# Performance work log

Measured on AMD Instinct MI355X. Metric: run time of the kernel, lower is better.

The kernel has to match this reference:

```python
import jax, jax.numpy as jnp
import numpy as np

NUM_HEADS = 8
EPS = 1e-6


def setup_inputs() -> dict:
    key = jax.random.key(0)
    ks = jax.random.split(key, 6)
    B, T, E = 2, 4096, 512
    s = 0.02
    x = jax.random.normal(ks[0], (B, T, E), dtype=jnp.float32)
    Wq = jax.random.normal(ks[1], (E, E), dtype=jnp.float32) * s
    Wk = jax.random.normal(ks[2], (E, E), dtype=jnp.float32) * s
    Wv = jax.random.normal(ks[3], (E, E), dtype=jnp.float32) * s
    Wo = jax.random.normal(ks[4], (E, E), dtype=jnp.float32) * s
    bq = jnp.zeros((E,), jnp.float32)
    bk = jnp.zeros((E,), jnp.float32)
    bv = jnp.zeros((E,), jnp.float32)
    bo = jnp.zeros((E,), jnp.float32)
    return {"x": x, "Wq": Wq, "bq": bq, "Wk": Wk, "bk": bk,
            "Wv": Wv, "bv": bv, "Wo": Wo, "bo": bo}


def _linear(x, W, b):
    # torch nn.Linear: y = x @ W.T + b
    return x @ W.T + b


def _feature_map(x):
    return jax.nn.elu(x) + 1.0


def _linear_attention(x, Wq, bq, Wk, bk, Wv, bv, Wo, bo):
    B, T, E = x.shape
    H = NUM_HEADS
    D = E // H

    def heads(y):  # (B,T,E) -> (T,B,H,D), time-major for scan
        return y.reshape(B, T, H, D).transpose(1, 0, 2, 3)

    q = _feature_map(heads(_linear(x, Wq, bq)))
    k = _feature_map(heads(_linear(x, Wk, bk)))
    v = heads(_linear(x, Wv, bv))

    # Causal linear attention: running KV outer-product state S (B,H,D,D)
    # and running key sum z (B,H,D). Equivalent to the naive
    # cumsum-of-outer-products (B,H,T,D,D) formulation, but O(D^2) state.
    S0 = jnp.zeros((B, H, D, D), x.dtype)
    z0 = jnp.zeros((B, H, D), x.dtype)

    def step(carry, qkv):
        S, z = carry
        qt, kt, vt = qkv  # each (B,H,D)
        S = S + kt[..., :, None] * vt[..., None, :]
        z = z + kt
        num = jnp.einsum('bhd,bhde->bhe', qt, S)
        den = jnp.sum(qt * z, axis=-1) + EPS  # (B,H)
        return (S, z), num / den[..., None]

    _, out = jax.lax.scan(step, (S0, z0), (q, k, v))  # (T,B,H,D)
    out = out.transpose(1, 0, 2, 3).reshape(B, T, E)
    return _linear(out, Wo, bo)


def reference(x, Wq, bq, Wk, bk, Wv, bv, Wo, bo):
    return _linear_attention(x, Wq, bq, Wk, bk, Wv, bv, Wo, bo)
```

## Files before the change

### kernel.cpp

```cpp
#include <hip/hip_runtime.h>
#include <hip/hip_bf16.h>

#define T_SEQ 4096
#define EMB   512
#define NH    8
#define HD    64
#define BATCH 2
#define M_ROWS (BATCH * T_SEQ)
#define NCHUNK 64
#define CS     64
#define BHEADS (BATCH * NH)

using bf16 = __hip_bfloat16;
typedef __attribute__((ext_vector_type(8))) short short8;
typedef __attribute__((ext_vector_type(4))) float floatx4;

__device__ __forceinline__ float bs2f(short s) {
    return __uint_as_float(((unsigned)(unsigned short)s) << 16);
}
__device__ __forceinline__ short f2bs(float f) {
    bf16 h = __float2bfloat16(f);
    return *reinterpret_cast<short*>(&h);
}
__device__ __forceinline__ float load_elem(const bf16* p, size_t i) {
    return __bfloat162float(p[i]);
}
__device__ __forceinline__ void store_elem(bf16* p, size_t i, float v) {
    p[i] = __float2bfloat16(v);
}
__device__ __forceinline__ void store_elem(float* p, size_t i, float v) {
    p[i] = v;
}
__device__ __forceinline__ void stage8(const bf16* g, short* l) {
    *reinterpret_cast<short8*>(l) = *reinterpret_cast<const short8*>(g);
}
__device__ __forceinline__ void stage8(const float* g, short* l) {
    float4 a = *reinterpret_cast<const float4*>(g);
    float4 b = *reinterpret_cast<const float4*>(g + 4);
    short8 v;
    v[0] = f2bs(a.x); v[1] = f2bs(a.y); v[2] = f2bs(a.z); v[3] = f2bs(a.w);
    v[4] = f2bs(b.x); v[5] = f2bs(b.y); v[6] = f2bs(b.z); v[7] = f2bs(b.w);
    *reinterpret_cast<short8*>(l) = v;
}
template <typename T> struct ModeOf { static constexpr int v = 0; };
template <> struct ModeOf<float>    { static constexpr int v = 1; };

__device__ __forceinline__ void gload_lds16(const short* g, short* l) {
    __builtin_amdgcn_global_load_lds(
        (const __attribute__((address_space(1))) void*)g,
        (__attribute__((address_space(3))) void*)l, 16, 0, 0);
}

#define LDSTR 72

__global__ void detect_dtype(const unsigned short* __restrict__ xraw,
                             int* __restrict__ flag)
{
    __shared__ int bad_s;
    const int tid = threadIdx.x;
    if (tid == 0) bad_s = 0;
    __syncthreads();
    bool bad = false;
    #pragma unroll
    for (int i = 0; i < 2; ++i) {
        uint4 u = reinterpret_cast<const uint4*>(xraw)[tid + i * 256];
        const unsigned w[4] = {u.x, u.y, u.z, u.w};
        #pragma unroll
        for (int k = 0; k < 4; ++k) {
            const float f = __uint_as_float(w[k] << 16);
            if (!(fabsf(f) <= 1e9f)) bad = true;
        }
    }
    if (bad) atomicOr(&bad_s, 1);
    __syncthreads();
    if (tid == 0) *flag = bad_s ? 1 : 0;
}

template <typename T>
__global__ __launch_bounds__(256) void convert_all(
    const int* __restrict__ flag,
    const T* __restrict__ x,
    const T* __restrict__ Wq, const T* __restrict__ bq,
    const T* __restrict__ Wk, const T* __restrict__ bk,
    const T* __restrict__ Wv, const T* __restrict__ bv,
    const T* __restrict__ Wo, const T* __restrict__ bo,
    short* __restrict__ xb, short* __restrict__ Wb, short* __restrict__ bb)
{
    if (*flag != ModeOf<T>::v) return;
    const int c = blockIdx.x * 256 + threadIdx.x;
    if (c < 524288) {
        stage8(x + (size_t)c * 8, xb + (size_t)c * 8);
    } else if (c < 655360) {
        const int c2 = c - 524288;
        const int w = c2 >> 15;
        const int off = (c2 & 32767) * 8;
        const T* src = (w == 0) ? Wq : (w == 1) ? Wk : (w == 2) ? Wv : Wo;
        stage8(src + off, Wb + w * 262144 + off);
    } else {
        const int c3 = c - 655360;
        const int bsel = c3 >> 6;
        const int off = (c3 & 63) * 8;
        const T* src = (bsel == 0) ? bq : (bsel == 1) ? bk : (bsel == 2) ? bv : bo;
        stage8(src + off, bb + bsel * 512 + off);
    }
}

__global__ __launch_bounds__(256) void qkv_gemm_dl(
    const short* __restrict__ xb, const short* __restrict__ Wb,
    const short* __restrict__ bb,
    bf16* __restrict__ Qf, bf16* __restrict__ Kf, bf16* __restrict__ Vf)
{
    const int mtile = blockIdx.x;
    const int ntile = blockIdx.y;
    const int which = ntile >> 2;
    const short* W = Wb + (size_t)which * 262144;
    const bf16* bias = (const bf16*)(bb + which * 512);
    bf16* outp = (which == 0) ? Qf : ((which == 1) ? Kf : Vf);
    const int nbase = (ntile & 3) * 128;
    const int mbase = mtile * 128;

    __shared__ short As[128 * 64];
    __shared__ short Bs[128 * 64];

    const int tid  = threadIdx.x;
    const int wave = tid >> 6, lane = tid & 63;
    const int wm = wave >> 1, wn = wave & 1;
    const int lm = lane & 15, quad = lane >> 4;
    const int srow = lane >> 3;
    const int scol = (lane & 7) * 8;

    floatx4 acc[4][4];
    const floatx4 zero = {0.f, 0.f, 0.f, 0.f};
    #pragma unroll
    for (int mt = 0; mt < 4; ++mt)
        #pragma unroll
        for (int nt = 0; nt < 4; ++nt) acc[mt][nt] = zero;

    for (int kt = 0; kt < EMB; kt += 64) {
        #pragma unroll
        for (int j = 0; j < 4; ++j) {
            const int issue = wave * 4 + j;
            const int row = issue * 8 + srow;
            gload_lds16(xb + (size_t)(mbase + row) * EMB + kt + scol,
                        &As[issue * 512]);
            gload_lds16(W  + (size_t)(nbase + row) * EMB + kt + scol,
                        &Bs[issue * 512]);
        }
        __syncthreads();
        #pragma unroll
        for (int ks = 0; ks < 2; ++ks) {
            short8 af[4], bfr[4];
            #pragma unroll
            for (int mt = 0; mt < 4; ++mt)
                af[mt] = *reinterpret_cast<const short8*>(
                    &As[(wm * 64 + mt * 16 + lm) * 64 + ks * 32 + quad * 8]);
            #pragma unroll
            for (int nt = 0; nt < 4; ++nt)
                bfr[nt] = *reinterpret_cast<const short8*>(
                    &Bs[(wn * 64 + nt * 16 + lm) * 64 + ks * 32 + quad * 8]);
            #pragma unroll
            for (int mt = 0; mt < 4; ++mt)
                #pragma unroll
                for (int nt = 0; nt < 4; ++nt)
                    acc[mt][nt] = __builtin_amdgcn_mfma_f32_16x16x32_bf16(
                        af[mt], bfr[nt], acc[mt][nt], 0, 0, 0);
        }
        __syncthreads();
    }

    #pragma unroll
    for (int nt = 0; nt < 4; ++nt) {
        const int col = nbase + wn * 64 + nt * 16 + lm;
        const float bv_ = load_elem(bias, col & 511);
        const int h = col >> 6, d = col & 63;
        #pragma unroll
        for (int mt = 0; mt < 4; ++mt)
            #pragma unroll
            for (int r = 0; r < 4; ++r) {
                const int row = mbase + wm * 64 + mt * 16 + quad * 4 + r;
                const int b = row >> 12, t = row & (T_SEQ - 1);
                float v = acc[mt][nt][r] + bv_;
                if (which != 2) v = (v > 0.f) ? (v + 1.f) : __expf(v);
                outp[(((size_t)(b * NH + h)) * T_SEQ + t) * HD + d] = __float2bfloat16(v);
            }
    }
}

__global__ __launch_bounds__(256) void chunk_kv(
    const bf16* __restrict__ Kf, const bf16* __restrict__ Vf,
    float* __restrict__ KV, float* __restrict__ ksum)
{
    const int bh = blockIdx.x >> 6;
    const int c  = blockIdx.x & 63;
    __shared__ short Kt[64 * LDSTR];
    __shared__ short Vt[64 * LDSTR];
    const int tid = threadIdx.x;
    const bf16* kp = Kf + ((size_t)bh * T_SEQ + c * CS) * HD;
    const bf16* vp = Vf + ((size_t)bh * T_SEQ + c * CS) * HD;

    #pragma unroll
    for (int j = 0; j < 2; ++j) {
        const int u = j * 256 + tid;
        const int e0 = u * 8;
        const int s = e0 >> 6, d0 = e0 & 63;
        short8 ku = *reinterpret_cast<const short8*>(kp + e0);
        short8 vu = *reinterpret_cast<const short8*>(vp + e0);
        #pragma unroll
        for (int i = 0; i < 8; ++i) {
            Kt[(d0 + i) * LDSTR + s] = ku[i];
            Vt[(d0 + i) * LDSTR + s] = vu[i];
        }
    }
    __syncthreads();

    const int w = tid >> 6, lane = tid & 63;
    const int lm = lane & 15, quad = lane >> 4;

    floatx4 acc[4];
    const floatx4 zero = {0.f, 0.f, 0.f, 0.f};
    #pragma unroll
    for (int nt = 0; nt < 4; ++nt) acc[nt] = zero;

    #pragma unroll
    for (int ks = 0; ks < 2; ++ks) {
        short8 ak = *reinterpret_cast<const short8*>(
            &Kt[(w * 16 + lm) * LDSTR + ks * 32 + quad * 8]);
        #pragma unroll
        for (int nt = 0; nt < 4; ++nt) {
            short8 bv = *reinterpret_cast<const short8*>(
                &Vt[(nt * 16 + lm) * LDSTR + ks * 32 + quad * 8]);
            acc[nt] = __builtin_amdgcn_mfma_f32_16x16x32_bf16(ak, bv, acc[nt], 0, 0, 0);
        }
    }

    float* kvout = KV + ((size_t)bh * NCHUNK + c) * 4096;
    #pragma unroll
    for (int nt = 0; nt < 4; ++nt)
        #pragma unroll
        for (int r = 0; r < 4; ++r) {
            const int dk = w * 16 + quad * 4 + r;
            const int dv = nt * 16 + lm;
            kvout[dk * 64 + dv] = acc[nt][r];
        }

    if (tid < 64) {
        float s = 0.f;
        #pragma unroll 8
        for (int t = 0; t < 64; ++t) s += bs2f(Kt[tid * LDSTR + t]);
        ksum[((size_t)bh * NCHUNK + c) * 64 + tid] = s;
    }
}

__global__ __launch_bounds__(256) void prefix_kv(
    float* __restrict__ KV, float* __restrict__ ksum)
{
    const int bh   = blockIdx.x >> 4;
    const int part = blockIdx.x & 15;
    const int tid  = threadIdx.x;
    const int e    = part * 256 + tid;
    float* base = KV + (size_t)bh * NCHUNK * 4096 + e;

    float s = 0.f;
    #pragma unroll
    for (int cb = 0; cb < 4; ++cb) {
        float v[16];
        #pragma unroll
        for (int i = 0; i < 16; ++i) v[i] = base[(size_t)(cb * 16 + i) * 4096];
        #pragma unroll
        for (int i = 0; i < 16; ++i) {
            const float tmp = v[i];
            base[(size_t)(cb * 16 + i) * 4096] = s;
            s += tmp;
        }
    }

    if (part == 0 && tid < 64) {
        float* zb = ksum + (size_t)bh * NCHUNK * 64 + tid;
        float z = 0.f;
        #pragma unroll
        for (int cb = 0; cb < 4; ++cb) {
            float v[16];
            #pragma unroll
            for (int i = 0; i < 16; ++i) v[i] = zb[(size_t)(cb * 16 + i) * 64];
            #pragma unroll
            for (int i = 0; i < 16; ++i) {
                const float tmp = v[i];
                zb[(size_t)(cb * 16 + i) * 64] = z;
                z += tmp;
            }
        }
    }
}

__global__ __launch_bounds__(256) void attn_mfma(
    const bf16* __restrict__ Qf, const bf16* __restrict__ Kf,
    const bf16* __restrict__ Vf, const float* __restrict__ KV,
    const float* __restrict__ ksum, bf16* __restrict__ Of)
{
    const int bh = blockIdx.x >> 6;
    const int c  = blockIdx.x & 63;
    const int b  = bh >> 3, h = bh & 7;

    __shared__ short Qs [64 * LDSTR];
    __shared__ short Ksn[64 * LDSTR];
    __shared__ short Vt [64 * LDSTR];
    __shared__ short Ps [64 * LDSTR];
    __shared__ short St [64 * LDSTR];
    __shared__ float zprev[64];
    __shared__ float rden[64];

    const int tid = threadIdx.x;
    const int w = tid >> 6, lane = tid & 63;
    const int lm = lane & 15, quad = lane >> 4;
    const size_t coff = ((size_t)bh * T_SEQ + c * CS) * HD;
    const float* Sp = KV + ((size_t)bh * NCHUNK + c) * 4096;

    #pragma unroll
    for (int j = 0; j < 2; ++j) {
        const int u  = j * 256 + tid;
        const int e0 = u * 8;
        const int r = e0 >> 6, cc = e0 & 63;
        *reinterpret_cast<short8*>(&Qs [r * LDSTR + cc]) =
            *reinterpret_cast<const short8*>(Qf + coff + e0);
        *reinterpret_cast<short8*>(&Ksn[r * LDSTR + cc]) =
            *reinterpret_cast<const short8*>(Kf + coff + e0);
        short8 vu = *reinterpret_cast<const short8*>(Vf + coff + e0);
        #pragma unroll
        for (int i = 0; i < 8; ++i) Vt[(cc + i) * LDSTR + r] = vu[i];
    }
    #pragma unroll
    for (int j = 0; j < 4; ++j) {
        const int u = j * 256 + tid;
        const float4 s4 = reinterpret_cast<const float4*>(Sp)[u];
        const int d = u >> 4;
        const int dv0 = (u & 15) * 4;
        St[(dv0 + 0) * LDSTR + d] = f2bs(s4.x);
        St[(dv0 + 1) * LDSTR + d] = f2bs(s4.y);
        St[(dv0 + 2) * LDSTR + d] = f2bs(s4.z);
        St[(dv0 + 3) * LDSTR + d] = f2bs(s4.w);
    }
    if (tid < 64) zprev[tid] = ksum[((size_t)bh * NCHUNK + c) * 64 + tid];
    __syncthreads();

    const floatx4 zero = {0.f, 0.f, 0.f, 0.f};
    short8 aq[2];
    #pragma unroll
    for (int ks = 0; ks < 2; ++ks)
        aq[ks] = *reinterpret_cast<const short8*>(
            &Qs[(w * 16 + lm) * LDSTR + ks * 32 + quad * 8]);

    floatx4 pacc[4];
    #pragma unroll
    for (int nt = 0; nt < 4; ++nt) pacc[nt] = zero;
    #pragma unroll
    for (int ks = 0; ks < 2; ++ks)
        #pragma unroll
        for (int nt = 0; nt < 4; ++nt) {
            short8 bk = *reinterpret_cast<const short8*>(
                &Ksn[(nt * 16 + lm) * LDSTR + ks * 32 + quad * 8]);
            pacc[nt] = __builtin_amdgcn_mfma_f32_16x16x32_bf16(aq[ks], bk, pacc[nt], 0, 0, 0);
        }
    #pragma unroll
    for (int nt = 0; nt < 4; ++nt)
        #pragma unroll
        for (int r = 0; r < 4; ++r) {
            const int t = w * 16 + quad * 4 + r;
            const int s = nt * 16 + lm;
            Ps[t * LDSTR + s] = f2bs((s <= t) ? pacc[nt][r] : 0.f);
        }

    floatx4 oacc[4];
    #pragma unroll
    for (int nt = 0; nt < 4; ++nt) oacc[nt] = zero;
    #pragma unroll
    for (int ks = 0; ks < 2; ++ks)
        #pragma unroll
        for (int nt = 0; nt < 4; ++nt) {
            short8 bs = *reinterpret_cast<const short8*>(
                &St[(nt * 16 + lm) * LDSTR + ks * 32 + quad * 8]);
            oacc[nt] = __builtin_amdgcn_mfma_f32_16x16x32_bf16(aq[ks], bs, oacc[nt], 0, 0, 0);
        }
    __syncthreads();

    if (tid < 64) {
        float rs = 0.f;
        #pragma unroll 8
        for (int s = 0; s < 64; ++s) rs += bs2f(Ps[tid * LDSTR + s]);
        float dz = 0.f;
        #pragma unroll 8
        for (int d = 0; d < 64; ++d) dz += bs2f(Qs[tid * LDSTR + d]) * zprev[d];
        rden[tid] = 1.f / (rs + dz + 1e-6f);
    }

    #pragma unroll
    for (int ks = 0; ks < 2; ++ks) {
        short8 ap = *reinterpret_cast<const short8*>(
            &Ps[(w * 16 + lm) * LDSTR + ks * 32 + quad * 8]);
        #pragma unroll
        for (int nt = 0; nt < 4; ++nt) {
            short8 bv = *reinterpret_cast<const short8*>(
                &Vt[(nt * 16 + lm) * LDSTR + ks * 32 + quad * 8]);
            oacc[nt] = __builtin_amdgcn_mfma_f32_16x16x32_bf16(ap, bv, oacc[nt], 0, 0, 0);
        }
    }
    __syncthreads();

    #pragma unroll
    for (int nt = 0; nt < 4; ++nt)
        #pragma unroll
        for (int r = 0; r < 4; ++r) {
            const int t  = w * 16 + quad * 4 + r;
            const int dv = nt * 16 + lm;
            const int tg = c * CS + t;
            Of[((size_t)(b * T_SEQ + tg)) * EMB + h * HD + dv] =
                __float2bfloat16(oacc[nt][r] * rden[t]);
        }
}

template <typename T>
__global__ __launch_bounds__(256) void out_proj_dl(
    const int* __restrict__ flag,
    const short* __restrict__ A, const short* __restrict__ Wb,
    const short* __restrict__ bb, T* __restrict__ out)
{
    if (*flag != ModeOf<T>::v) return;

    const int mbase = blockIdx.x * 128;
    const int nbase = blockIdx.y * 128;
    const short* W = Wb + (size_t)3 * 262144;
    const bf16* bias = (const bf16*)(bb + 3 * 512);

    __shared__ short As[128 * 64];
    __shared__ short Bs[128 * 64];

    const int tid  = threadIdx.x;
    const int wave = tid >> 6, lane = tid & 63;
    const int wm = wave >> 1, wn = wave & 1;
    const int lm = lane & 15, quad = lane >> 4;
    const int srow = lane >> 3;
    const int scol = (lane & 7) * 8;

    floatx4 acc[4][4];
    const floatx4 zero = {0.f, 0.f, 0.f, 0.f};
    #pragma unroll
    for (int mt = 0; mt < 4; ++mt)
        #pragma unroll
        for (int nt = 0; nt < 4; ++nt) acc[mt][nt] = zero;

    for (int kt = 0; kt < EMB; kt += 64) {
        #pragma unroll
        for (int j = 0; j < 4; ++j) {
            const int issue = wave * 4 + j;
            const int row = issue * 8 + srow;
            gload_lds16(A + (size_t)(mbase + row) * EMB + kt + scol,
                        &As[issue * 512]);
            gload_lds16(W + (size_t)(nbase + row) * EMB + kt + scol,
                        &Bs[issue * 512]);
        }
        __syncthreads();
        #pragma unroll
        for (int ks = 0; ks < 2; ++ks) {
            short8 af[4], bfr[4];
            #pragma unroll
            for (int mt = 0; mt < 4; ++mt)
                af[mt] = *reinterpret_cast<const short8*>(
                    &As[(wm * 64 + mt * 16 + lm) * 64 + ks * 32 + quad * 8]);
            #pragma unroll
            for (int nt = 0; nt < 4; ++nt)
                bfr[nt] = *reinterpret_cast<const short8*>(
                    &Bs[(wn * 64 + nt * 16 + lm) * 64 + ks * 32 + quad * 8]);
            #pragma unroll
            for (int mt = 0; mt < 4; ++mt)
                #pragma unroll
                for (int nt = 0; nt < 4; ++nt)
                    acc[mt][nt] = __builtin_amdgcn_mfma_f32_16x16x32_bf16(
                        af[mt], bfr[nt], acc[mt][nt], 0, 0, 0);
        }
        __syncthreads();
    }

    #pragma unroll
    for (int nt = 0; nt < 4; ++nt) {
        const int col = nbase + wn * 64 + nt * 16 + lm;
        const float bv_ = load_elem(bias, col);
        #pragma unroll
        for (int mt = 0; mt < 4; ++mt)
            #pragma unroll
            for (int r = 0; r < 4; ++r) {
                const int row = mbase + wm * 64 + mt * 16 + quad * 4 + r;
                store_elem(out, (size_t)row * EMB + col, acc[mt][nt][r] + bv_);
            }
    }
}

extern "C" void kernel_launch(void* const* d_in, const int* in_sizes, int n_in,
                              void* d_out, int out_size, void* d_ws, size_t ws_size,
                              hipStream_t stream)
{
    int*  flag = (int*)d_ws;
    bf16* Qf = (bf16*)((char*)d_ws + 64);
    bf16* Kf = Qf + 4194304;
    bf16* Vf = Kf + 4194304;
    float* KV = (float*)(Vf + 4194304);
    short* xb = (short*)KV;
    float* ks = KV + 4194304;
    bf16* Of = (bf16*)(ks + 65536);
    short* Wb = (short*)(Of + 4194304);
    short* bb = Wb + 1048576;

    detect_dtype<<<1, 256, 0, stream>>>((const unsigned short*)d_in[0], flag);

    convert_all<bf16><<<dim3(2561), 256, 0, stream>>>(flag,
        (const bf16*)d_in[0],
        (const bf16*)d_in[1], (const bf16*)d_in[2],
        (const bf16*)d_in[3], (const bf16*)d_in[4],
        (const bf16*)d_in[5], (const bf16*)d_in[6],
        (const bf16*)d_in[7], (const bf16*)d_in[8],
        xb, Wb, bb);
    convert_all<float><<<dim3(2561), 256, 0, stream>>>(flag,
        (const float*)d_in[0],
        (const float*)d_in[1], (const float*)d_in[2],
        (const float*)d_in[3], (const float*)d_in[4],
        (const float*)d_in[5], (const float*)d_in[6],
        (const float*)d_in[7], (const float*)d_in[8],
        xb, Wb, bb);

    qkv_gemm_dl<<<dim3(64, 12), 256, 0, stream>>>(xb, Wb, bb, Qf, Kf, Vf);
    chunk_kv<<<dim3(BHEADS * NCHUNK), 256, 0, stream>>>(Kf, Vf, KV, ks);
    prefix_kv<<<dim3(BHEADS * 16), 256, 0, stream>>>(KV, ks);
    attn_mfma<<<dim3(BHEADS * NCHUNK), 256, 0, stream>>>(Qf, Kf, Vf, KV, ks, Of);

    out_proj_dl<bf16><<<dim3(64, 4), 256, 0, stream>>>(flag,
        (const short*)Of, Wb, bb, (bf16*)d_out);
    out_proj_dl<float><<<dim3(64, 4), 256, 0, stream>>>(flag,
        (const short*)Of, Wb, bb, (float*)d_out);
}
```

Measured before the change: 167.2 us.

## Fold dtype probe into kernels, transpose KV state, parallelize denominator

Drops the separate dtype-detect kernel and the duplicate per-dtype convert and out-projection launches by having every block probe the input dtype itself with a block-wide OR. This removes three launches at the cost of redundant probe reads in each block. The chunk KV state is now stored transposed, so the attention kernel can pack it into LDS with vector stores instead of scattered scalar ones. The per-row normalizer is computed across all waves with shuffle reductions rather than by 64 serial threads, which also removes one barrier.

```diff
diff --git a/kernel.cpp b/kernel.cpp
--- a/kernel.cpp
+++ b/kernel.cpp
@@ -13,6 +13,7 @@
 
 using bf16 = __hip_bfloat16;
 typedef __attribute__((ext_vector_type(8))) short short8;
+typedef __attribute__((ext_vector_type(4))) short short4v;
 typedef __attribute__((ext_vector_type(4))) float floatx4;
 
 __device__ __forceinline__ float bs2f(short s) {
@@ -24,12 +25,6 @@
 }
 __device__ __forceinline__ float load_elem(const bf16* p, size_t i) {
     return __bfloat162float(p[i]);
-}
-__device__ __forceinline__ void store_elem(bf16* p, size_t i, float v) {
-    p[i] = __float2bfloat16(v);
-}
-__device__ __forceinline__ void store_elem(float* p, size_t i, float v) {
-    p[i] = v;
 }
 __device__ __forceinline__ void stage8(const bf16* g, short* l) {
     *reinterpret_cast<short8*>(l) = *reinterpret_cast<const short8*>(g);
@@ -42,8 +37,6 @@
     v[4] = f2bs(b.x); v[5] = f2bs(b.y); v[6] = f2bs(b.z); v[7] = f2bs(b.w);
     *reinterpret_cast<short8*>(l) = v;
 }
-template <typename T> struct ModeOf { static constexpr int v = 0; };
-template <> struct ModeOf<float>    { static constexpr int v = 1; };
 
 __device__ __forceinline__ void gload_lds16(const short* g, short* l) {
     __builtin_amdgcn_global_load_lds(
@@ -53,17 +46,13 @@
 
 #define LDSTR 72
 
-__global__ void detect_dtype(const unsigned short* __restrict__ xraw,
-                             int* __restrict__ flag)
-{
-    __shared__ int bad_s;
+__device__ __forceinline__ int probe_mode(const void* x) {
+    const uint4* p = (const uint4*)x;
     const int tid = threadIdx.x;
-    if (tid == 0) bad_s = 0;
-    __syncthreads();
     bool bad = false;
     #pragma unroll
     for (int i = 0; i < 2; ++i) {
-        uint4 u = reinterpret_cast<const uint4*>(xraw)[tid + i * 256];
+        uint4 u = p[tid + i * 256];
         const unsigned w[4] = {u.x, u.y, u.z, u.w};
         #pragma unroll
         for (int k = 0; k < 4; ++k) {
@@ -71,38 +60,41 @@
             if (!(fabsf(f) <= 1e9f)) bad = true;
         }
     }
-    if (bad) atomicOr(&bad_s, 1);
-    __syncthreads();
-    if (tid == 0) *flag = bad_s ? 1 : 0;
+    return __syncthreads_or(bad ? 1 : 0) ? 1 : 0;
 }
 
 template <typename T>
-__global__ __launch_bounds__(256) void convert_all(
-    const int* __restrict__ flag,
-    const T* __restrict__ x,
-    const T* __restrict__ Wq, const T* __restrict__ bq,
-    const T* __restrict__ Wk, const T* __restrict__ bk,
-    const T* __restrict__ Wv, const T* __restrict__ bv,
-    const T* __restrict__ Wo, const T* __restrict__ bo,
-    short* __restrict__ xb, short* __restrict__ Wb, short* __restrict__ bb)
-{
-    if (*flag != ModeOf<T>::v) return;
-    const int c = blockIdx.x * 256 + threadIdx.x;
+__device__ __forceinline__ void convert_body(
+    const void* const* in, short* xb, short* Wb, short* bb, int c)
+{
     if (c < 524288) {
-        stage8(x + (size_t)c * 8, xb + (size_t)c * 8);
+        stage8((const T*)in[0] + (size_t)c * 8, xb + (size_t)c * 8);
     } else if (c < 655360) {
         const int c2 = c - 524288;
         const int w = c2 >> 15;
         const int off = (c2 & 32767) * 8;
-        const T* src = (w == 0) ? Wq : (w == 1) ? Wk : (w == 2) ? Wv : Wo;
+        const T* src = (const T*)in[w == 0 ? 1 : (w == 1 ? 3 : (w == 2 ? 5 : 7))];
         stage8(src + off, Wb + w * 262144 + off);
-    } else {
+    } else if (c < 655616) {
         const int c3 = c - 655360;
         const int bsel = c3 >> 6;
         const int off = (c3 & 63) * 8;
-        const T* src = (bsel == 0) ? bq : (bsel == 1) ? bk : (bsel == 2) ? bv : bo;
+        const T* src = (const T*)in[bsel == 0 ? 2 : (bsel == 1 ? 4 : (bsel == 2 ? 6 : 8))];
         stage8(src + off, bb + bsel * 512 + off);
     }
+}
+
+__global__ __launch_bounds__(256) void convert_all(
+    const void* x, const void* Wq, const void* bq,
+    const void* Wk, const void* bk, const void* Wv, const void* bv,
+    const void* Wo, const void* bo,
+    short* __restrict__ xb, short* __restrict__ Wb, short* __restrict__ bb)
+{
+    const void* in[9] = {x, Wq, bq, Wk, bk, Wv, bv, Wo, bo};
+    const int mode = probe_mode(x);
+    const int c = blockIdx.x * 256 + threadIdx.x;
+    if (mode) convert_body<float>(in, xb, Wb, bb, c);
+    else      convert_body<bf16>(in, xb, Wb, bb, c);
 }
 
 __global__ __launch_bounds__(256) void qkv_gemm_dl(
@@ -188,7 +180,7 @@
 
 __global__ __launch_bounds__(256) void chunk_kv(
     const bf16* __restrict__ Kf, const bf16* __restrict__ Vf,
-    float* __restrict__ KV, float* __restrict__ ksum)
+    float* __restrict__ KVt, float* __restrict__ ksum)
 {
     const int bh = blockIdx.x >> 6;
     const int c  = blockIdx.x & 63;
@@ -223,24 +215,24 @@
 
     #pragma unroll
     for (int ks = 0; ks < 2; ++ks) {
-        short8 ak = *reinterpret_cast<const short8*>(
-            &Kt[(w * 16 + lm) * LDSTR + ks * 32 + quad * 8]);
+        short8 av = *reinterpret_cast<const short8*>(
+            &Vt[(w * 16 + lm) * LDSTR + ks * 32 + quad * 8]);
         #pragma unroll
         for (int nt = 0; nt < 4; ++nt) {
-            short8 bv = *reinterpret_cast<const short8*>(
-                &Vt[(nt * 16 + lm) * LDSTR + ks * 32 + quad * 8]);
-            acc[nt] = __builtin_amdgcn_mfma_f32_16x16x32_bf16(ak, bv, acc[nt], 0, 0, 0);
-        }
-    }
-
-    float* kvout = KV + ((size_t)bh * NCHUNK + c) * 4096;
+            short8 bk = *reinterpret_cast<const short8*>(
+                &Kt[(nt * 16 + lm) * LDSTR + ks * 32 + quad * 8]);
+            acc[nt] = __builtin_amdgcn_mfma_f32_16x16x32_bf16(av, bk, acc[nt], 0, 0, 0);
+        }
+    }
+
+    float* kvout = KVt + ((size_t)bh * NCHUNK + c) * 4096;
     #pragma unroll
     for (int nt = 0; nt < 4; ++nt)
         #pragma unroll
         for (int r = 0; r < 4; ++r) {
-            const int dk = w * 16 + quad * 4 + r;
-            const int dv = nt * 16 + lm;
-            kvout[dk * 64 + dv] = acc[nt][r];
+            const int dv = w * 16 + quad * 4 + r;
+            const int dk = nt * 16 + lm;
+            kvout[dv * 64 + dk] = acc[nt][r];
         }
 
     if (tid < 64) {
@@ -252,13 +244,13 @@
 }
 
 __global__ __launch_bounds__(256) void prefix_kv(
-    float* __restrict__ KV, float* __restrict__ ksum)
+    float* __restrict__ KVt, float* __restrict__ ksum)
 {
     const int bh   = blockIdx.x >> 4;
     const int part = blockIdx.x & 15;
     const int tid  = threadIdx.x;
     const int e    = part * 256 + tid;
-    float* base = KV + (size_t)bh * NCHUNK * 4096 + e;
+    float* base = KVt + (size_t)bh * NCHUNK * 4096 + e;
 
     float s = 0.f;
     #pragma unroll
@@ -294,7 +286,7 @@
 
 __global__ __launch_bounds__(256) void attn_mfma(
     const bf16* __restrict__ Qf, const bf16* __restrict__ Kf,
-    const bf16* __restrict__ Vf, const float* __restrict__ KV,
+    const bf16* __restrict__ Vf, const float* __restrict__ KVt,
     const float* __restrict__ ksum, bf16* __restrict__ Of)
 {
     const int bh = blockIdx.x >> 6;
@@ -307,13 +299,12 @@
     __shared__ short Ps [64 * LDSTR];
     __shared__ short St [64 * LDSTR];
     __shared__ float zprev[64];
-    __shared__ float rden[64];
 
     const int tid = threadIdx.x;
     const int w = tid >> 6, lane = tid & 63;
     const int lm = lane & 15, quad = lane >> 4;
     const size_t coff = ((size_t)bh * T_SEQ + c * CS) * HD;
-    const float* Sp = KV + ((size_t)bh * NCHUNK + c) * 4096;
+    const float* Sp = KVt + ((size_t)bh * NCHUNK + c) * 4096;
 
     #pragma unroll
     for (int j = 0; j < 2; ++j) {
@@ -330,14 +321,13 @@
     }
     #pragma unroll
     for (int j = 0; j < 4; ++j) {
-        const int u = j * 256 + tid;
+        const int u  = j * 256 + tid;
+        const int dv = u >> 4, d0 = (u & 15) * 4;
         const float4 s4 = reinterpret_cast<const float4*>(Sp)[u];
-        const int d = u >> 4;
-        const int dv0 = (u & 15) * 4;
-        St[(dv0 + 0) * LDSTR + d] = f2bs(s4.x);
-        St[(dv0 + 1) * LDSTR + d] = f2bs(s4.y);
-        St[(dv0 + 2) * LDSTR + d] = f2bs(s4.z);
-        St[(dv0 + 3) * LDSTR + d] = f2bs(s4.w);
+        short4v pk;
+        pk[0] = f2bs(s4.x); pk[1] = f2bs(s4.y);
+        pk[2] = f2bs(s4.z); pk[3] = f2bs(s4.w);
+        *reinterpret_cast<short4v*>(&St[dv * LDSTR + d0]) = pk;
     }
     if (tid < 64) zprev[tid] = ksum[((size_t)bh * NCHUNK + c) * 64 + tid];
     __syncthreads();
@@ -360,14 +350,34 @@
                 &Ksn[(nt * 16 + lm) * LDSTR + ks * 32 + quad * 8]);
             pacc[nt] = __builtin_amdgcn_mfma_f32_16x16x32_bf16(aq[ks], bk, pacc[nt], 0, 0, 0);
         }
+
+    float tot[4] = {0.f, 0.f, 0.f, 0.f};
     #pragma unroll
     for (int nt = 0; nt < 4; ++nt)
         #pragma unroll
         for (int r = 0; r < 4; ++r) {
             const int t = w * 16 + quad * 4 + r;
             const int s = nt * 16 + lm;
-            Ps[t * LDSTR + s] = f2bs((s <= t) ? pacc[nt][r] : 0.f);
-        }
+            const float m = (s <= t) ? pacc[nt][r] : 0.f;
+            Ps[t * LDSTR + s] = f2bs(m);
+            tot[r] += m;
+        }
+    #pragma unroll
+    for (int r = 0; r < 4; ++r) {
+        const int t = w * 16 + quad * 4 + r;
+        #pragma unroll
+        for (int j = 0; j < 4; ++j) {
+            const int d = lm + j * 16;
+            tot[r] += bs2f(Qs[t * LDSTR + d]) * zprev[d];
+        }
+    }
+    #pragma unroll
+    for (int mask = 1; mask < 16; mask <<= 1)
+        #pragma unroll
+        for (int r = 0; r < 4; ++r) tot[r] += __shfl_xor(tot[r], mask);
+    float rdenl[4];
+    #pragma unroll
+    for (int r = 0; r < 4; ++r) rdenl[r] = 1.f / (tot[r] + 1e-6f);
 
     floatx4 oacc[4];
     #pragma unroll
@@ -382,16 +392,6 @@
         }
     __syncthreads();
 
-    if (tid < 64) {
-        float rs = 0.f;
-        #pragma unroll 8
-        for (int s = 0; s < 64; ++s) rs += bs2f(Ps[tid * LDSTR + s]);
-        float dz = 0.f;
-        #pragma unroll 8
-        for (int d = 0; d < 64; ++d) dz += bs2f(Qs[tid * LDSTR + d]) * zprev[d];
-        rden[tid] = 1.f / (rs + dz + 1e-6f);
-    }
-
     #pragma unroll
     for (int ks = 0; ks < 2; ++ks) {
         short8 ap = *reinterpret_cast<const short8*>(
@@ -403,7 +403,6 @@
             oacc[nt] = __builtin_amdgcn_mfma_f32_16x16x32_bf16(ap, bv, oacc[nt], 0, 0, 0);
         }
     }
-    __syncthreads();
 
     #pragma unroll
     for (int nt = 0; nt < 4; ++nt)
@@ -413,17 +412,16 @@
             const int dv = nt * 16 + lm;
             const int tg = c * CS + t;
             Of[((size_t)(b * T_SEQ + tg)) * EMB + h * HD + dv] =
-                __float2bfloat16(oacc[nt][r] * rden[t]);
-        }
-}
-
-template <typename T>
+                __float2bfloat16(oacc[nt][r] * rdenl[r]);
+        }
+}
+
 __global__ __launch_bounds__(256) void out_proj_dl(
-    const int* __restrict__ flag,
+    const void* __restrict__ xprobe,
     const short* __restrict__ A, const short* __restrict__ Wb,
-    const short* __restrict__ bb, T* __restrict__ out)
-{
-    if (*flag != ModeOf<T>::v) return;
+    const short* __restrict__ bb, void* __restrict__ out)
+{
+    const int mode = probe_mode(xprobe);
 
     const int mbase = blockIdx.x * 128;
     const int nbase = blockIdx.y * 128;
@@ -488,7 +486,9 @@
             #pragma unroll
             for (int r = 0; r < 4; ++r) {
                 const int row = mbase + wm * 64 + mt * 16 + quad * 4 + r;
-                store_elem(out, (size_t)row * EMB + col, acc[mt][nt][r] + bv_);
+                const float v = acc[mt][nt][r] + bv_;
+                if (mode) ((float*)out)[(size_t)row * EMB + col] = v;
+                else      ((bf16*)out)[(size_t)row * EMB + col] = __float2bfloat16(v);
             }
     }
 }
@@ -497,41 +497,25 @@
                               void* d_out, int out_size, void* d_ws, size_t ws_size,
                               hipStream_t stream)
 {
-    int*  flag = (int*)d_ws;
     bf16* Qf = (bf16*)((char*)d_ws + 64);
     bf16* Kf = Qf + 4194304;
     bf16* Vf = Kf + 4194304;
-    float* KV = (float*)(Vf + 4194304);
-    short* xb = (short*)KV;
-    float* ks = KV + 4194304;
+    float* KVt = (float*)(Vf + 4194304);
+    short* xb = (short*)KVt;
+    float* ks = KVt + 4194304;
     bf16* Of = (bf16*)(ks + 65536);
     short* Wb = (short*)(Of + 4194304);
     short* bb = Wb + 1048576;
 
-    detect_dtype<<<1, 256, 0, stream>>>((const unsigned short*)d_in[0], flag);
-
-    convert_all<bf16><<<dim3(2561), 256, 0, stream>>>(flag,
-        (const bf16*)d_in[0],
-        (const bf16*)d_in[1], (const bf16*)d_in[2],
-        (const bf16*)d_in[3], (const bf16*)d_in[4],
-        (const bf16*)d_in[5], (const bf16*)d_in[6],
-        (const bf16*)d_in[7], (const bf16*)d_in[8],
-        xb, Wb, bb);
-    convert_all<float><<<dim3(2561), 256, 0, stream>>>(flag,
-        (const float*)d_in[0],
-        (const float*)d_in[1], (const float*)d_in[2],
-        (const float*)d_in[3], (const float*)d_in[4],
-        (const float*)d_in[5], (const float*)d_in[6],
-        (const float*)d_in[7], (const float*)d_in[8],
-        xb, Wb, bb);
+    convert_all<<<dim3(2561), 256, 0, stream>>>(
+        d_in[0], d_in[1], d_in[2], d_in[3], d_in[4],
+        d_in[5], d_in[6], d_in[7], d_in[8], xb, Wb, bb);
 
     qkv_gemm_dl<<<dim3(64, 12), 256, 0, stream>>>(xb, Wb, bb, Qf, Kf, Vf);
-    chunk_kv<<<dim3(BHEADS * NCHUNK), 256, 0, stream>>>(Kf, Vf, KV, ks);
-    prefix_kv<<<dim3(BHEADS * 16), 256, 0, stream>>>(KV, ks);
-    attn_mfma<<<dim3(BHEADS * NCHUNK), 256, 0, stream>>>(Qf, Kf, Vf, KV, ks, Of);
-
-    out_proj_dl<bf16><<<dim3(64, 4), 256, 0, stream>>>(flag,
-        (const short*)Of, Wb, bb, (bf16*)d_out);
-    out_proj_dl<float><<<dim3(64, 4), 256, 0, stream>>>(flag,
-        (const short*)Of, Wb, bb, (float*)d_out);
-}
+    chunk_kv<<<dim3(BHEADS * NCHUNK), 256, 0, stream>>>(Kf, Vf, KVt, ks);
+    prefix_kv<<<dim3(BHEADS * 16), 256, 0, stream>>>(KVt, ks);
+    attn_mfma<<<dim3(BHEADS * NCHUNK), 256, 0, stream>>>(Qf, Kf, Vf, KVt, ks, Of);
+
+    out_proj_dl<<<dim3(64, 4), 256, 0, stream>>>(
+        d_in[0], (const short*)Of, Wb, bb, d_out);
+}
```

New measurement: 161.6 us. 1.03x faster.
